# Kernel optimization log

Measured on AMD Instinct MI355X. Metric: run time of the kernel, lower is better.

Reference implementation:

```python
import jax, jax.numpy as jnp
import numpy as np

DIM = 1024
NUM_HEADS = 16
HEAD_DIM = DIM // NUM_HEADS  # 64
LATENT = 128
Q_RANK = 256
B, S = 4, 2048


def setup_inputs() -> dict:
    key = jax.random.key(0)
    ks = jax.random.split(key, 12)
    w = lambda k, shape: jax.random.normal(k, shape, dtype=jnp.float32) * 0.02
    x = jax.random.normal(ks[0], (B, S, DIM), dtype=jnp.float32)
    mask = jnp.tril(jnp.ones((S, S), dtype=jnp.int32))[None, None, :, :]  # causal [1,1,S,S]
    return {
        "x": x,
        "mask": mask,
        "w_kvc": w(ks[1], (DIM, LATENT)),   "b_kvc": jnp.zeros((LATENT,), jnp.float32),
        "w_kvu": w(ks[2], (LATENT, 2 * DIM)), "b_kvu": jnp.zeros((2 * DIM,), jnp.float32),
        "w_qc":  w(ks[3], (DIM, Q_RANK)),   "b_qc": jnp.zeros((Q_RANK,), jnp.float32),
        "w_qu":  w(ks[4], (Q_RANK, DIM)),   "b_qu": jnp.zeros((DIM,), jnp.float32),
        "w_o":   w(ks[5], (DIM, DIM)),      "b_o": jnp.zeros((DIM,), jnp.float32),
    }


def reference(x, mask, w_kvc, b_kvc, w_kvu, b_kvu, w_qc, b_qc, w_qu, b_qu, w_o, b_o):
    b, s, _ = x.shape
    # low-rank KV path
    kv_latent = x @ w_kvc + b_kvc                      # [B,S,latent]
    kv_up = kv_latent @ w_kvu + b_kvu                  # [B,S,2*dim]
    K, V = jnp.split(kv_up, 2, axis=-1)                # each [B,S,dim]
    # low-rank Q path
    Q = (x @ w_qc + b_qc) @ w_qu + b_qu                # [B,S,dim]

    def split_heads(t):  # [B,S,dim] -> [B,H,S,hd]
        return t.reshape(b, s, NUM_HEADS, HEAD_DIM).transpose(0, 2, 1, 3)

    Qh, Kh, Vh = split_heads(Q), split_heads(K), split_heads(V)
    scores = jnp.einsum("bhsd,bhtd->bhst", Qh, Kh) / np.sqrt(HEAD_DIM).astype(np.float32)
    scores = jnp.where(mask == 0, jnp.float32(-1e9), scores)
    attn = jax.nn.softmax(scores, axis=-1)
    ctx = jnp.einsum("bhst,bhtd->bhsd", attn, Vh)      # [B,H,S,hd]
    ctx = ctx.transpose(0, 2, 1, 3).reshape(b, s, DIM)
    return ctx @ w_o + b_o
```

## Files before the change

kernel.cpp:

```cpp
#include <hip/hip_runtime.h>

typedef __attribute__((ext_vector_type(8))) short short8;
typedef __attribute__((ext_vector_type(4))) float f32x4;

#define DIM 1024
#define NH 16
#define HD 64
#define LAT 128
#define QR 256
#define NCAT (LAT + QR)
#define BB 4
#define SS 2048
#define BS (BB * SS)

#define SCALE_LOG2E 0.18033688011112042f

__device__ __forceinline__ unsigned short f2b(float f) {
  unsigned int u = __builtin_bit_cast(unsigned int, f);
  u += 0x7FFFu + ((u >> 16) & 1u);
  return (unsigned short)(u >> 16);
}
__device__ __forceinline__ float b2f(unsigned short h) {
  unsigned int u = ((unsigned int)h) << 16;
  return __builtin_bit_cast(float, u);
}
__device__ __forceinline__ unsigned int pack_bf16_pair(float f0, float f1) {
  unsigned int u0 = __builtin_bit_cast(unsigned int, f0) + 0x8000u;
  unsigned int u1 = __builtin_bit_cast(unsigned int, f1) + 0x8000u;
  return __builtin_amdgcn_perm(u1, u0, 0x07060302u);
}
__device__ __forceinline__ void gll16(const unsigned short* g, unsigned short* l) {
  __builtin_amdgcn_global_load_lds(
      (const __attribute__((address_space(1))) unsigned int*)g,
      (__attribute__((address_space(3))) unsigned int*)l, 16, 0, 0);
}

__global__ __launch_bounds__(256) void cvt_x(const float* __restrict__ in,
                                             unsigned short* __restrict__ out, int n4) {
  int i = blockIdx.x * 256 + threadIdx.x;
  if (i >= n4) return;
  f32x4 v = ((const f32x4*)in)[i];
  ushort4 o;
  o.x = f2b(v[0]); o.y = f2b(v[1]); o.z = f2b(v[2]); o.w = f2b(v[3]);
  ((ushort4*)out)[i] = o;
}

__global__ __launch_bounds__(256) void prep_weights(
    const float* __restrict__ w_kvc, const float* __restrict__ w_qc,
    const float* __restrict__ w_kvu, const float* __restrict__ w_qu,
    const float* __restrict__ w_o, const float* __restrict__ b_kvc,
    const float* __restrict__ b_qc, unsigned short* __restrict__ wcatT,
    unsigned short* __restrict__ wkvuT, unsigned short* __restrict__ wquT,
    unsigned short* __restrict__ woT, float* __restrict__ bias_cat) {
  __shared__ unsigned short T[64 * 72];
  const int id = blockIdx.x;
  const int tid = threadIdx.x;
  if (id >= 480) {
    if (tid < LAT) bias_cat[tid] = b_kvc[tid];
    else bias_cat[tid] = b_qc[tid - LAT];
    if (tid < 128) bias_cat[tid + 256] = b_qc[tid + 128];
    return;
  }
  const float* in; unsigned short* out; int K, N, tile;
  if (id < 32)       { in = w_kvc; out = wcatT;                       K = DIM; N = LAT;     tile = id; }
  else if (id < 96)  { in = w_qc;  out = wcatT + (size_t)LAT * DIM;   K = DIM; N = QR;      tile = id - 32; }
  else if (id < 160) { in = w_kvu; out = wkvuT;                       K = LAT; N = 2 * DIM; tile = id - 96; }
  else if (id < 224) { in = w_qu;  out = wquT;                        K = QR;  N = DIM;     tile = id - 160; }
  else               { in = w_o;   out = woT;                         K = DIM; N = DIM;     tile = id - 224; }
  const int ktiles = K >> 6;
  const int k0 = (tile % ktiles) * 64, n0 = (tile / ktiles) * 64;
  {
    const int r = tid >> 2, cq = (tid & 3) * 16;
#pragma unroll
    for (int j = 0; j < 4; ++j) {
      f32x4 v = *(const f32x4*)(in + (size_t)(k0 + r) * N + n0 + cq + j * 4);
      ushort4 o;
      o.x = f2b(v[0]); o.y = f2b(v[1]); o.z = f2b(v[2]); o.w = f2b(v[3]);
      *(ushort4*)(T + r * 72 + cq + j * 4) = o;
    }
  }
  __syncthreads();
#pragma unroll
  for (int s = 0; s < 2; ++s) {
    int idx = tid + s * 256;
    int nr = idx >> 3, kg = (idx & 7) * 8;
    short8 o;
#pragma unroll
    for (int i = 0; i < 8; i++) o[i] = T[(kg + i) * 72 + nr];
    *(short8*)(out + (size_t)(n0 + nr) * K + k0 + kg) = o;
  }
}

__global__ __launch_bounds__(256) void transpose_v(const unsigned short* __restrict__ KVb,
                                                   unsigned short* __restrict__ VTb) {
  __shared__ unsigned short T[64 * 72];
  const int tid = threadIdx.x;
  const int st = blockIdx.x, dt = blockIdx.y, b = blockIdx.z;
  const int s0 = st * 64, d0 = dt * 64;
#pragma unroll
  for (int t = 0; t < 2; ++t) {
    int idx = tid + t * 256;
    int r = idx >> 3, c = idx & 7;
    short8 v = *(const short8*)(KVb + (size_t)(b * SS + s0 + r) * (2 * DIM) + DIM + d0 + c * 8);
    *(short8*)(T + r * 72 + c * 8) = v;
  }
  __syncthreads();
#pragma unroll
  for (int t = 0; t < 2; ++t) {
    int idx = tid + t * 256;
    int dr = idx >> 3, cg = idx & 7;
    short8 o;
#pragma unroll
    for (int i = 0; i < 8; i++) o[i] = T[(cg * 8 + i) * 72 + dr];
    *(short8*)(VTb + (size_t)(b * DIM + d0 + dr) * SS + s0 + cg * 8) = o;
  }
}

__global__ __launch_bounds__(256, 4) void gemm_lds(const unsigned short* __restrict__ A,
                                                   const unsigned short* __restrict__ WT,
                                                   const float* __restrict__ bias,
                                                   float* __restrict__ outF,
                                                   unsigned short* __restrict__ outB,
                                                   int N, int K, int lda, int ldout,
                                                   float scale, int nblk) {
  __shared__ unsigned short As[128 * 64];
  __shared__ unsigned short Bs[128 * 64];
  const int tid = threadIdx.x;
  const int wave = tid >> 6, lane = tid & 63;
  const int ln = lane & 15, quad = lane >> 4;
  const int chunk = nblk >> 3;
  const int sw = (blockIdx.x & 7) * chunk + (blockIdx.x >> 3);
  const int nwx = N >> 7;
  const int bx = sw % nwx, by = sw / nwx;
  const int m0 = by * 128, n0 = bx * 128;
  const int wm = (wave >> 1) * 64, wn = (wave & 1) * 64;

  const int srow = wave * 32 + (lane >> 3);
  const int scol = (lane & 7) * 8;
  const unsigned short* Ag = A + (size_t)(m0 + srow) * lda + scol;
  const unsigned short* Bg = WT + (size_t)(n0 + srow) * K + scol;
  unsigned short* Al = As + wave * 32 * 64;
  unsigned short* Bl = Bs + wave * 32 * 64;

  f32x4 acc[4][4];
#pragma unroll
  for (int i = 0; i < 4; i++)
#pragma unroll
    for (int j = 0; j < 4; j++) acc[i][j] = (f32x4){0.f, 0.f, 0.f, 0.f};

  for (int k0 = 0; k0 < K; k0 += 64) {
    __syncthreads();
#pragma unroll
    for (int i = 0; i < 4; i++) {
      gll16(Ag + (size_t)i * 8 * lda + k0, Al + i * 8 * 64);
      gll16(Bg + (size_t)i * 8 * K + k0, Bl + i * 8 * 64);
    }
    __syncthreads();
#pragma unroll
    for (int kc = 0; kc < 2; kc++) {
      short8 af[4], bf[4];
#pragma unroll
      for (int i = 0; i < 4; i++) {
        af[i] = *(const short8*)(As + (wm + i * 16 + ln) * 64 + kc * 32 + quad * 8);
        bf[i] = *(const short8*)(Bs + (wn + i * 16 + ln) * 64 + kc * 32 + quad * 8);
      }
#pragma unroll
      for (int mi = 0; mi < 4; mi++)
#pragma unroll
        for (int ni = 0; ni < 4; ni++)
          acc[mi][ni] =
              __builtin_amdgcn_mfma_f32_16x16x32_bf16(af[mi], bf[ni], acc[mi][ni], 0, 0, 0);
    }
  }

#pragma unroll
  for (int mi = 0; mi < 4; mi++) {
    const int row = m0 + wm + mi * 16 + quad * 4;
#pragma unroll
    for (int ni = 0; ni < 4; ni++) {
      const int col = n0 + wn + ni * 16 + ln;
      const float bv = bias[col];
#pragma unroll
      for (int r = 0; r < 4; r++) {
        float v = (acc[mi][ni][r] + bv) * scale;
        size_t o = (size_t)(row + r) * ldout + col;
        if (outF) outF[o] = v;
        if (outB) outB[o] = f2b(v);
      }
    }
  }
}

__global__ __launch_bounds__(256, 4) void attn_mfma(const unsigned short* __restrict__ Qb,
                                                    const unsigned short* __restrict__ KVb,
                                                    const unsigned short* __restrict__ VTb,
                                                    unsigned short* __restrict__ ctxB) {
  __shared__ unsigned short smem[(64 + 64) * 72 + 4 * 16 * 72];
  unsigned short* Ks = smem;
  unsigned short* Vts = smem + 64 * 72;
  unsigned short* Ps = smem + 128 * 72;
  const int tid = threadIdx.x;
  const int wave = tid >> 6, lane = tid & 63;
  const int ln = lane & 15, quad = lane >> 4;
  const int hw = blockIdx.x;
  const int xcd = hw & 7, slot = hw >> 3;
  const int grp = xcd * 8 + (slot >> 4);
  const int pair = slot & 15;
  const int h = grp & 15, b = grp >> 4;
  const int tA = pair, tB = 31 - pair;
  const int s0A = tA * 64, s0B = tB * 64;
  const int ktmaxB = tB;
  const int qminA = s0A + wave * 16, qmaxA = qminA + 15;
  const int qminB = s0B + wave * 16, qmaxB = qminB + 15;

  short8 qfA[2], qfB[2];
  {
    const unsigned short* qa =
        Qb + (size_t)(b * SS + s0A + wave * 16 + ln) * DIM + h * HD + quad * 8;
    qfA[0] = *(const short8*)qa;
    qfA[1] = *(const short8*)(qa + 32);
    const unsigned short* qb2 =
        Qb + (size_t)(b * SS + s0B + wave * 16 + ln) * DIM + h * HD + quad * 8;
    qfB[0] = *(const short8*)qb2;
    qfB[1] = *(const short8*)(qb2 + 32);
  }

  f32x4 ocA[4], ocB[4];
  float lpA = 0.f, lpB = 0.f;
#pragma unroll
  for (int i = 0; i < 4; i++) {
    ocA[i] = (f32x4){0.f, 0.f, 0.f, 0.f};
    ocB[i] = (f32x4){0.f, 0.f, 0.f, 0.f};
  }

  unsigned short* Pw = Ps + wave * (16 * 72);

  const int srow = tid >> 3, sc8 = (tid & 7) * 8;

  const unsigned short* kptr =
      KVb + (size_t)(b * SS + srow) * (2 * DIM) + h * HD + sc8;
  const unsigned short* vptr = VTb + (size_t)(b * DIM + h * HD + srow) * SS + sc8;
  const size_t kstep = (size_t)64 * 2 * DIM;
  const size_t krow32 = (size_t)32 * 2 * DIM;
  const size_t vrow32 = (size_t)32 * SS;

  short8 kreg0 = *(const short8*)kptr;
  short8 kreg1 = *(const short8*)(kptr + krow32);
  short8 vreg0 = *(const short8*)vptr;
  short8 vreg1 = *(const short8*)(vptr + vrow32);

  for (int kt = 0; kt <= ktmaxB; ++kt) {
    __syncthreads();
    *(short8*)(Ks + srow * 72 + sc8) = kreg0;
    *(short8*)(Ks + (srow + 32) * 72 + sc8) = kreg1;
    *(short8*)(Vts + srow * 72 + sc8) = vreg0;
    *(short8*)(Vts + (srow + 32) * 72 + sc8) = vreg1;
    __syncthreads();
    if (kt < ktmaxB) {
      kptr += kstep; vptr += 64;
      kreg0 = *(const short8*)kptr;
      kreg1 = *(const short8*)(kptr + krow32);
      vreg0 = *(const short8*)vptr;
      vreg1 = *(const short8*)(vptr + vrow32);
    }

    const int k0g = kt * 64;

    auto stream = [&](const short8* qf, f32x4* oc, float& lp, const int qminw,
                      const int qmaxw) {
      if (k0g > qmaxw) return;
      const bool needmask = (k0g + 63 > qminw);

      f32x4 sacc[4];
#pragma unroll
      for (int nt = 0; nt < 4; nt++) sacc[nt] = (f32x4){0.f, 0.f, 0.f, 0.f};
      __builtin_amdgcn_s_setprio(1);
#pragma unroll
      for (int kc = 0; kc < 2; kc++) {
#pragma unroll
        for (int nt = 0; nt < 4; nt++) {
          if (k0g + nt * 16 > qmaxw) continue;
          short8 kfrag = *(const short8*)(Ks + (nt * 16 + ln) * 72 + kc * 32 + quad * 8);
          sacc[nt] =
              __builtin_amdgcn_mfma_f32_16x16x32_bf16(kfrag, qf[kc], sacc[nt], 0, 0, 0);
        }
      }
      __builtin_amdgcn_s_setprio(0);

      const int qg = qminw + ln;
      float lt = 0.f;
      if (!needmask) {
#pragma unroll
        for (int nt = 0; nt < 4; nt++) {
          float p0 = __builtin_exp2f(sacc[nt][0]);
          float p1 = __builtin_exp2f(sacc[nt][1]);
          float p2 = __builtin_exp2f(sacc[nt][2]);
          float p3 = __builtin_exp2f(sacc[nt][3]);
          uint2 pw;
          pw.x = pack_bf16_pair(p0, p1);
          pw.y = pack_bf16_pair(p2, p3);
          *(uint2*)(Pw + ln * 72 + nt * 16 + quad * 4) = pw;
          lt += (p0 + p1) + (p2 + p3);
        }
      } else {
#pragma unroll
        for (int nt = 0; nt < 4; nt++) {
          const int base = k0g + nt * 16 + quad * 4;
          float pe[4];
#pragma unroll
          for (int r = 0; r < 4; r++) {
            float p = __builtin_exp2f(sacc[nt][r]);
            if (base + r > qg) p = 0.f;
            pe[r] = p;
          }
          uint2 pw;
          pw.x = pack_bf16_pair(pe[0], pe[1]);
          pw.y = pack_bf16_pair(pe[2], pe[3]);
          *(uint2*)(Pw + ln * 72 + nt * 16 + quad * 4) = pw;
          lt += (pe[0] + pe[1]) + (pe[2] + pe[3]);
        }
      }
      lp += lt;

      __builtin_amdgcn_s_setprio(1);
#pragma unroll
      for (int kc = 0; kc < 2; kc++) {
        if (k0g + kc * 32 > qmaxw) continue;
        short8 pfrag = *(const short8*)(Pw + ln * 72 + kc * 32 + quad * 8);
#pragma unroll
        for (int dt = 0; dt < 4; dt++) {
          short8 vfrag = *(const short8*)(Vts + (dt * 16 + ln) * 72 + kc * 32 + quad * 8);
          oc[dt] =
              __builtin_amdgcn_mfma_f32_16x16x32_bf16(pfrag, vfrag, oc[dt], 0, 0, 0);
        }
      }
      __builtin_amdgcn_s_setprio(0);
    };

    stream(qfA, ocA, lpA, qminA, qmaxA);
    stream(qfB, ocB, lpB, qminB, qmaxB);
  }

  lpA += __shfl_xor(lpA, 16, 64);
  lpA += __shfl_xor(lpA, 32, 64);
  lpB += __shfl_xor(lpB, 16, 64);
  lpB += __shfl_xor(lpB, 32, 64);
  float liA[4], liB[4];
#pragma unroll
  for (int r = 0; r < 4; r++) {
    liA[r] = 1.f / __shfl(lpA, quad * 4 + r, 64);
    liB[r] = 1.f / __shfl(lpB, quad * 4 + r, 64);
  }

  __syncthreads();
#pragma unroll
  for (int r = 0; r < 4; r++) {
#pragma unroll
    for (int dt = 0; dt < 4; dt++)
      smem[(wave * 16 + quad * 4 + r) * 72 + dt * 16 + ln] = f2b(ocA[dt][r] * liA[r]);
  }
  __syncthreads();
#pragma unroll
  for (int t = 0; t < 2; ++t) {
    int idx = tid + t * 256;
    int row = idx >> 3, c = idx & 7;
    short8 v = *(const short8*)(smem + row * 72 + c * 8);
    *(short8*)(ctxB + (size_t)(b * SS + s0A + row) * DIM + h * HD + c * 8) = v;
  }
  __syncthreads();
#pragma unroll
  for (int r = 0; r < 4; r++) {
#pragma unroll
    for (int dt = 0; dt < 4; dt++)
      smem[(wave * 16 + quad * 4 + r) * 72 + dt * 16 + ln] = f2b(ocB[dt][r] * liB[r]);
  }
  __syncthreads();
#pragma unroll
  for (int t = 0; t < 2; ++t) {
    int idx = tid + t * 256;
    int row = idx >> 3, c = idx & 7;
    short8 v = *(const short8*)(smem + row * 72 + c * 8);
    *(short8*)(ctxB + (size_t)(b * SS + s0B + row) * DIM + h * HD + c * 8) = v;
  }
}

extern "C" void kernel_launch(void* const* d_in, const int* in_sizes, int n_in,
                              void* d_out, int out_size, void* d_ws, size_t ws_size,
                              hipStream_t stream) {
  const float* x     = (const float*)d_in[0];
  const float* w_kvc = (const float*)d_in[2];
  const float* b_kvc = (const float*)d_in[3];
  const float* w_kvu = (const float*)d_in[4];
  const float* b_kvu = (const float*)d_in[5];
  const float* w_qc  = (const float*)d_in[6];
  const float* b_qc  = (const float*)d_in[7];
  const float* w_qu  = (const float*)d_in[8];
  const float* b_qu  = (const float*)d_in[9];
  const float* w_o   = (const float*)d_in[10];
  const float* b_o   = (const float*)d_in[11];
  float* out = (float*)d_out;

  unsigned short* xb     = (unsigned short*)d_ws;
  unsigned short* wcatT  = xb + (size_t)BS * DIM;
  unsigned short* wkvuT  = wcatT + (size_t)NCAT * DIM;
  unsigned short* wquT   = wkvuT + (size_t)LAT * 2 * DIM;
  unsigned short* woT    = wquT + (size_t)QR * DIM;
  unsigned short* kvqlat = woT + (size_t)DIM * DIM;
  unsigned short* kvup   = kvqlat + (size_t)BS * NCAT;
  unsigned short* Qbuf   = kvup + (size_t)BS * 2 * DIM;
  unsigned short* ctx    = Qbuf + (size_t)BS * DIM;
  float* bias_cat        = (float*)(ctx + (size_t)BS * DIM);

  cvt_x<<<(BS * DIM / 4 + 255) / 256, 256, 0, stream>>>(x, xb, BS * DIM / 4);
  prep_weights<<<481, 256, 0, stream>>>(w_kvc, w_qc, w_kvu, w_qu, w_o, b_kvc, b_qc,
                                        wcatT, wkvuT, wquT, woT, bias_cat);

  gemm_lds<<<dim3(BS / 128 * (NCAT / 128)), 256, 0, stream>>>(
      xb, wcatT, bias_cat, nullptr, kvqlat, NCAT, DIM, DIM, NCAT, 1.0f,
      BS / 128 * (NCAT / 128));
  gemm_lds<<<dim3(BS / 128 * (2 * DIM / 128)), 256, 0, stream>>>(
      kvqlat, wkvuT, b_kvu, nullptr, kvup, 2 * DIM, LAT, NCAT, 2 * DIM, 1.0f,
      BS / 128 * (2 * DIM / 128));
  unsigned short* VT = xb;
  transpose_v<<<dim3(SS / 64, DIM / 64, BB), 256, 0, stream>>>(kvup, VT);
  gemm_lds<<<dim3(BS / 128 * (DIM / 128)), 256, 0, stream>>>(
      kvqlat + LAT, wquT, b_qu, nullptr, Qbuf, DIM, QR, NCAT, DIM, SCALE_LOG2E,
      BS / 128 * (DIM / 128));
  attn_mfma<<<dim3(32 * NH * BB / 2), 256, 0, stream>>>(Qbuf, kvup, VT, ctx);
  gemm_lds<<<dim3(BS / 128 * (DIM / 128)), 256, 0, stream>>>(
      ctx, woT, b_o, out, nullptr, DIM, DIM, DIM, DIM, 1.0f,
      BS / 128 * (DIM / 128));
}
```

Baseline: 278.8 us.

## Fuse V transpose into KV-up GEMM epilogue, interleave attention streams, swizzle LDS

The KV up-projection GEMM now writes V already transposed through shared memory in its epilogue, which removes the separate transpose kernel and its extra read and write of V. The attention kernel interleaves the two query tiles so each K and V fragment read from LDS feeds the MFMAs of both tiles. It also replaces padded LDS rows with an XOR-swizzled 64-wide layout to cut memory footprint and bank conflicts. Risks are higher register pressure from holding both score tiles at once, and the V half of the KV buffer is no longer written row-major (only the K half is read afterwards).

```diff
diff --git a/kernel.cpp b/kernel.cpp
--- a/kernel.cpp
+++ b/kernel.cpp
@@ -91,40 +91,17 @@
   }
 }
 
-__global__ __launch_bounds__(256) void transpose_v(const unsigned short* __restrict__ KVb,
-                                                   unsigned short* __restrict__ VTb) {
-  __shared__ unsigned short T[64 * 72];
-  const int tid = threadIdx.x;
-  const int st = blockIdx.x, dt = blockIdx.y, b = blockIdx.z;
-  const int s0 = st * 64, d0 = dt * 64;
-#pragma unroll
-  for (int t = 0; t < 2; ++t) {
-    int idx = tid + t * 256;
-    int r = idx >> 3, c = idx & 7;
-    short8 v = *(const short8*)(KVb + (size_t)(b * SS + s0 + r) * (2 * DIM) + DIM + d0 + c * 8);
-    *(short8*)(T + r * 72 + c * 8) = v;
-  }
-  __syncthreads();
-#pragma unroll
-  for (int t = 0; t < 2; ++t) {
-    int idx = tid + t * 256;
-    int dr = idx >> 3, cg = idx & 7;
-    short8 o;
-#pragma unroll
-    for (int i = 0; i < 8; i++) o[i] = T[(cg * 8 + i) * 72 + dr];
-    *(short8*)(VTb + (size_t)(b * DIM + d0 + dr) * SS + s0 + cg * 8) = o;
-  }
-}
-
 __global__ __launch_bounds__(256, 4) void gemm_lds(const unsigned short* __restrict__ A,
                                                    const unsigned short* __restrict__ WT,
                                                    const float* __restrict__ bias,
                                                    float* __restrict__ outF,
                                                    unsigned short* __restrict__ outB,
+                                                   unsigned short* __restrict__ vtOut,
                                                    int N, int K, int lda, int ldout,
                                                    float scale, int nblk) {
-  __shared__ unsigned short As[128 * 64];
-  __shared__ unsigned short Bs[128 * 64];
+  __shared__ unsigned short gsm[17408];
+  unsigned short* As = gsm;
+  unsigned short* Bs = gsm + 8192;
   const int tid = threadIdx.x;
   const int wave = tid >> 6, lane = tid & 63;
   const int ln = lane & 15, quad = lane >> 4;
@@ -173,6 +150,32 @@
     }
   }
 
+  if (vtOut && n0 >= DIM) {
+    __syncthreads();
+#pragma unroll
+    for (int mi = 0; mi < 4; mi++) {
+      const int s = wm + mi * 16 + quad * 4;
+#pragma unroll
+      for (int ni = 0; ni < 4; ni++) {
+        const int d = wn + ni * 16 + ln;
+        const float bv = bias[n0 + d];
+#pragma unroll
+        for (int r = 0; r < 4; r++)
+          gsm[d * 136 + s + r] = f2b(acc[mi][ni][r] + bv);
+      }
+    }
+    __syncthreads();
+    const int d0 = n0 - DIM, bb = m0 >> 11, s0l = m0 & (SS - 1);
+#pragma unroll
+    for (int t = 0; t < 8; ++t) {
+      int idx = tid + t * 256;
+      int dr = idx >> 4, cs = (idx & 15) * 8;
+      short8 v = *(const short8*)(gsm + dr * 136 + cs);
+      *(short8*)(vtOut + (size_t)(bb * DIM + d0 + dr) * SS + s0l + cs) = v;
+    }
+    return;
+  }
+
 #pragma unroll
   for (int mi = 0; mi < 4; mi++) {
     const int row = m0 + wm + mi * 16 + quad * 4;
@@ -195,10 +198,11 @@
                                                     const unsigned short* __restrict__ KVb,
                                                     const unsigned short* __restrict__ VTb,
                                                     unsigned short* __restrict__ ctxB) {
-  __shared__ unsigned short smem[(64 + 64) * 72 + 4 * 16 * 72];
+  __shared__ unsigned short smem[16384];
   unsigned short* Ks = smem;
-  unsigned short* Vts = smem + 64 * 72;
-  unsigned short* Ps = smem + 128 * 72;
+  unsigned short* Vts = smem + 4096;
+  unsigned short* PsA = smem + 8192;
+  unsigned short* PsB = smem + 12288;
   const int tid = threadIdx.x;
   const int wave = tid >> 6, lane = tid & 63;
   const int ln = lane & 15, quad = lane >> 4;
@@ -233,9 +237,12 @@
     ocB[i] = (f32x4){0.f, 0.f, 0.f, 0.f};
   }
 
-  unsigned short* Pw = Ps + wave * (16 * 72);
+  unsigned short* PwA = PsA + wave * (16 * 64);
+  unsigned short* PwB = PsB + wave * (16 * 64);
+  const int swz = (ln & 7) << 3;
 
   const int srow = tid >> 3, sc8 = (tid & 7) * 8;
+  const int ssc = sc8 ^ ((srow & 7) << 3);
 
   const unsigned short* kptr =
       KVb + (size_t)(b * SS + srow) * (2 * DIM) + h * HD + sc8;
@@ -251,10 +258,10 @@
 
   for (int kt = 0; kt <= ktmaxB; ++kt) {
     __syncthreads();
-    *(short8*)(Ks + srow * 72 + sc8) = kreg0;
-    *(short8*)(Ks + (srow + 32) * 72 + sc8) = kreg1;
-    *(short8*)(Vts + srow * 72 + sc8) = vreg0;
-    *(short8*)(Vts + (srow + 32) * 72 + sc8) = vreg1;
+    *(short8*)(Ks + srow * 64 + ssc) = kreg0;
+    *(short8*)(Ks + (srow + 32) * 64 + ssc) = kreg1;
+    *(short8*)(Vts + srow * 64 + ssc) = vreg0;
+    *(short8*)(Vts + (srow + 32) * 64 + ssc) = vreg1;
     __syncthreads();
     if (kt < ktmaxB) {
       kptr += kstep; vptr += 64;
@@ -265,41 +272,45 @@
     }
 
     const int k0g = kt * 64;
-
-    auto stream = [&](const short8* qf, f32x4* oc, float& lp, const int qminw,
-                      const int qmaxw) {
-      if (k0g > qmaxw) return;
-      const bool needmask = (k0g + 63 > qminw);
-
-      f32x4 sacc[4];
-#pragma unroll
-      for (int nt = 0; nt < 4; nt++) sacc[nt] = (f32x4){0.f, 0.f, 0.f, 0.f};
-      __builtin_amdgcn_s_setprio(1);
-#pragma unroll
-      for (int kc = 0; kc < 2; kc++) {
-#pragma unroll
-        for (int nt = 0; nt < 4; nt++) {
-          if (k0g + nt * 16 > qmaxw) continue;
-          short8 kfrag = *(const short8*)(Ks + (nt * 16 + ln) * 72 + kc * 32 + quad * 8);
-          sacc[nt] =
-              __builtin_amdgcn_mfma_f32_16x16x32_bf16(kfrag, qf[kc], sacc[nt], 0, 0, 0);
-        }
-      }
-      __builtin_amdgcn_s_setprio(0);
-
-      const int qg = qminw + ln;
+    const bool aAct = (k0g <= qmaxA);
+
+    f32x4 sA[4], sB[4];
+#pragma unroll
+    for (int nt = 0; nt < 4; nt++) {
+      sA[nt] = (f32x4){0.f, 0.f, 0.f, 0.f};
+      sB[nt] = (f32x4){0.f, 0.f, 0.f, 0.f};
+    }
+    __builtin_amdgcn_s_setprio(1);
+#pragma unroll
+    for (int kc = 0; kc < 2; kc++) {
+      const int rc = (kc * 32 + quad * 8) ^ swz;
+#pragma unroll
+      for (int nt = 0; nt < 4; nt++) {
+        if (k0g + nt * 16 > qmaxB) continue;
+        short8 kfrag = *(const short8*)(Ks + (nt * 16 + ln) * 64 + rc);
+        sB[nt] = __builtin_amdgcn_mfma_f32_16x16x32_bf16(kfrag, qfB[kc], sB[nt], 0, 0, 0);
+        if (aAct && k0g + nt * 16 <= qmaxA)
+          sA[nt] = __builtin_amdgcn_mfma_f32_16x16x32_bf16(kfrag, qfA[kc], sA[nt], 0, 0, 0);
+      }
+    }
+    __builtin_amdgcn_s_setprio(0);
+
+    const int pcs = (ln & 7) << 3;
+    {
+      const bool needmask = (k0g + 63 > qminB);
+      const int qg = qminB + ln;
       float lt = 0.f;
       if (!needmask) {
 #pragma unroll
         for (int nt = 0; nt < 4; nt++) {
-          float p0 = __builtin_exp2f(sacc[nt][0]);
-          float p1 = __builtin_exp2f(sacc[nt][1]);
-          float p2 = __builtin_exp2f(sacc[nt][2]);
-          float p3 = __builtin_exp2f(sacc[nt][3]);
+          float p0 = __builtin_exp2f(sB[nt][0]);
+          float p1 = __builtin_exp2f(sB[nt][1]);
+          float p2 = __builtin_exp2f(sB[nt][2]);
+          float p3 = __builtin_exp2f(sB[nt][3]);
           uint2 pw;
           pw.x = pack_bf16_pair(p0, p1);
           pw.y = pack_bf16_pair(p2, p3);
-          *(uint2*)(Pw + ln * 72 + nt * 16 + quad * 4) = pw;
+          *(uint2*)(PwB + ln * 64 + ((nt * 16 + quad * 4) ^ pcs)) = pw;
           lt += (p0 + p1) + (p2 + p3);
         }
       } else {
@@ -309,36 +320,76 @@
           float pe[4];
 #pragma unroll
           for (int r = 0; r < 4; r++) {
-            float p = __builtin_exp2f(sacc[nt][r]);
+            float p = __builtin_exp2f(sB[nt][r]);
             if (base + r > qg) p = 0.f;
             pe[r] = p;
           }
           uint2 pw;
           pw.x = pack_bf16_pair(pe[0], pe[1]);
           pw.y = pack_bf16_pair(pe[2], pe[3]);
-          *(uint2*)(Pw + ln * 72 + nt * 16 + quad * 4) = pw;
+          *(uint2*)(PwB + ln * 64 + ((nt * 16 + quad * 4) ^ pcs)) = pw;
           lt += (pe[0] + pe[1]) + (pe[2] + pe[3]);
         }
       }
-      lp += lt;
-
-      __builtin_amdgcn_s_setprio(1);
-#pragma unroll
-      for (int kc = 0; kc < 2; kc++) {
-        if (k0g + kc * 32 > qmaxw) continue;
-        short8 pfrag = *(const short8*)(Pw + ln * 72 + kc * 32 + quad * 8);
-#pragma unroll
-        for (int dt = 0; dt < 4; dt++) {
-          short8 vfrag = *(const short8*)(Vts + (dt * 16 + ln) * 72 + kc * 32 + quad * 8);
-          oc[dt] =
-              __builtin_amdgcn_mfma_f32_16x16x32_bf16(pfrag, vfrag, oc[dt], 0, 0, 0);
+      lpB += lt;
+    }
+    if (aAct) {
+      const bool needmask = (k0g + 63 > qminA);
+      const int qg = qminA + ln;
+      float lt = 0.f;
+      if (!needmask) {
+#pragma unroll
+        for (int nt = 0; nt < 4; nt++) {
+          float p0 = __builtin_exp2f(sA[nt][0]);
+          float p1 = __builtin_exp2f(sA[nt][1]);
+          float p2 = __builtin_exp2f(sA[nt][2]);
+          float p3 = __builtin_exp2f(sA[nt][3]);
+          uint2 pw;
+          pw.x = pack_bf16_pair(p0, p1);
+          pw.y = pack_bf16_pair(p2, p3);
+          *(uint2*)(PwA + ln * 64 + ((nt * 16 + quad * 4) ^ pcs)) = pw;
+          lt += (p0 + p1) + (p2 + p3);
         }
-      }
-      __builtin_amdgcn_s_setprio(0);
-    };
-
-    stream(qfA, ocA, lpA, qminA, qmaxA);
-    stream(qfB, ocB, lpB, qminB, qmaxB);
+      } else {
+#pragma unroll
+        for (int nt = 0; nt < 4; nt++) {
+          const int base = k0g + nt * 16 + quad * 4;
+          float pe[4];
+#pragma unroll
+          for (int r = 0; r < 4; r++) {
+            float p = __builtin_exp2f(sA[nt][r]);
+            if (base + r > qg) p = 0.f;
+            pe[r] = p;
+          }
+          uint2 pw;
+          pw.x = pack_bf16_pair(pe[0], pe[1]);
+          pw.y = pack_bf16_pair(pe[2], pe[3]);
+          *(uint2*)(PwA + ln * 64 + ((nt * 16 + quad * 4) ^ pcs)) = pw;
+          lt += (pe[0] + pe[1]) + (pe[2] + pe[3]);
+        }
+      }
+      lpA += lt;
+    }
+
+    __builtin_amdgcn_s_setprio(1);
+#pragma unroll
+    for (int kc = 0; kc < 2; kc++) {
+      const bool bPV = (k0g + kc * 32 <= qmaxB);
+      const bool aPV = aAct && (k0g + kc * 32 <= qmaxA);
+      if (!bPV) continue;
+      const int rc = (kc * 32 + quad * 8) ^ swz;
+      short8 pB = *(const short8*)(PwB + ln * 64 + rc);
+      short8 pA;
+      if (aPV) pA = *(const short8*)(PwA + ln * 64 + rc);
+#pragma unroll
+      for (int dt = 0; dt < 4; dt++) {
+        short8 vfrag = *(const short8*)(Vts + (dt * 16 + ln) * 64 + rc);
+        ocB[dt] = __builtin_amdgcn_mfma_f32_16x16x32_bf16(pB, vfrag, ocB[dt], 0, 0, 0);
+        if (aPV)
+          ocA[dt] = __builtin_amdgcn_mfma_f32_16x16x32_bf16(pA, vfrag, ocA[dt], 0, 0, 0);
+      }
+    }
+    __builtin_amdgcn_s_setprio(0);
   }
 
   lpA += __shfl_xor(lpA, 16, 64);
@@ -416,18 +467,17 @@
                                         wcatT, wkvuT, wquT, woT, bias_cat);
 
   gemm_lds<<<dim3(BS / 128 * (NCAT / 128)), 256, 0, stream>>>(
-      xb, wcatT, bias_cat, nullptr, kvqlat, NCAT, DIM, DIM, NCAT, 1.0f,
+      xb, wcatT, bias_cat, nullptr, kvqlat, nullptr, NCAT, DIM, DIM, NCAT, 1.0f,
       BS / 128 * (NCAT / 128));
+  unsigned short* VT = xb;
   gemm_lds<<<dim3(BS / 128 * (2 * DIM / 128)), 256, 0, stream>>>(
-      kvqlat, wkvuT, b_kvu, nullptr, kvup, 2 * DIM, LAT, NCAT, 2 * DIM, 1.0f,
+      kvqlat, wkvuT, b_kvu, nullptr, kvup, VT, 2 * DIM, LAT, NCAT, 2 * DIM, 1.0f,
       BS / 128 * (2 * DIM / 128));
-  unsigned short* VT = xb;
-  transpose_v<<<dim3(SS / 64, DIM / 64, BB), 256, 0, stream>>>(kvup, VT);
   gemm_lds<<<dim3(BS / 128 * (DIM / 128)), 256, 0, stream>>>(
-      kvqlat + LAT, wquT, b_qu, nullptr, Qbuf, DIM, QR, NCAT, DIM, SCALE_LOG2E,
+      kvqlat + LAT, wquT, b_qu, nullptr, Qbuf, nullptr, DIM, QR, NCAT, DIM, SCALE_LOG2E,
       BS / 128 * (DIM / 128));
   attn_mfma<<<dim3(32 * NH * BB / 2), 256, 0, stream>>>(Qbuf, kvup, VT, ctx);
   gemm_lds<<<dim3(BS / 128 * (DIM / 128)), 256, 0, stream>>>(
-      ctx, woT, b_o, out, nullptr, DIM, DIM, DIM, DIM, 1.0f,
+      ctx, woT, b_o, out, nullptr, nullptr, DIM, DIM, DIM, DIM, 1.0f,
       BS / 128 * (DIM / 128));
 }
```

Measured after the change: 577.9 us. 2.07x slower.

## Fuse V transpose into KV up-projection epilogue and swizzle attention LDS layout

Applied to the files above, without the earlier changes.

The KV up-projection GEMM now writes V tiles straight out in transposed layout through an LDS staging buffer in its epilogue, so the separate transpose_v kernel and its extra read of V from global memory are gone. V columns are no longer written to kvup, which is safe because attention reads V only from VT. The attention kernel also replaces padded LDS rows (stride 72) with unpadded rows (stride 64) plus an XOR swizzle on K, V and P tiles, shrinking shared memory while trying to avoid bank conflicts. The GEMM's shared-memory footprint grows to fit the transpose staging tile, which may reduce occupancy slightly.

```diff
diff --git a/kernel.cpp b/kernel.cpp
--- a/kernel.cpp
+++ b/kernel.cpp
@@ -91,40 +91,17 @@
   }
 }
 
-__global__ __launch_bounds__(256) void transpose_v(const unsigned short* __restrict__ KVb,
-                                                   unsigned short* __restrict__ VTb) {
-  __shared__ unsigned short T[64 * 72];
-  const int tid = threadIdx.x;
-  const int st = blockIdx.x, dt = blockIdx.y, b = blockIdx.z;
-  const int s0 = st * 64, d0 = dt * 64;
-#pragma unroll
-  for (int t = 0; t < 2; ++t) {
-    int idx = tid + t * 256;
-    int r = idx >> 3, c = idx & 7;
-    short8 v = *(const short8*)(KVb + (size_t)(b * SS + s0 + r) * (2 * DIM) + DIM + d0 + c * 8);
-    *(short8*)(T + r * 72 + c * 8) = v;
-  }
-  __syncthreads();
-#pragma unroll
-  for (int t = 0; t < 2; ++t) {
-    int idx = tid + t * 256;
-    int dr = idx >> 3, cg = idx & 7;
-    short8 o;
-#pragma unroll
-    for (int i = 0; i < 8; i++) o[i] = T[(cg * 8 + i) * 72 + dr];
-    *(short8*)(VTb + (size_t)(b * DIM + d0 + dr) * SS + s0 + cg * 8) = o;
-  }
-}
-
 __global__ __launch_bounds__(256, 4) void gemm_lds(const unsigned short* __restrict__ A,
                                                    const unsigned short* __restrict__ WT,
                                                    const float* __restrict__ bias,
                                                    float* __restrict__ outF,
                                                    unsigned short* __restrict__ outB,
+                                                   unsigned short* __restrict__ vtOut,
                                                    int N, int K, int lda, int ldout,
                                                    float scale, int nblk) {
-  __shared__ unsigned short As[128 * 64];
-  __shared__ unsigned short Bs[128 * 64];
+  __shared__ unsigned short gsm[17408];
+  unsigned short* As = gsm;
+  unsigned short* Bs = gsm + 8192;
   const int tid = threadIdx.x;
   const int wave = tid >> 6, lane = tid & 63;
   const int ln = lane & 15, quad = lane >> 4;
@@ -173,6 +150,32 @@
     }
   }
 
+  if (vtOut && n0 >= DIM) {
+    __syncthreads();
+#pragma unroll
+    for (int mi = 0; mi < 4; mi++) {
+      const int s = wm + mi * 16 + quad * 4;
+#pragma unroll
+      for (int ni = 0; ni < 4; ni++) {
+        const int d = wn + ni * 16 + ln;
+        const float bv = bias[n0 + d];
+#pragma unroll
+        for (int r = 0; r < 4; r++)
+          gsm[d * 136 + s + r] = f2b(acc[mi][ni][r] + bv);
+      }
+    }
+    __syncthreads();
+    const int d0 = n0 - DIM, bb = m0 >> 11, s0l = m0 & (SS - 1);
+#pragma unroll
+    for (int t = 0; t < 8; ++t) {
+      int idx = tid + t * 256;
+      int dr = idx >> 4, cs = (idx & 15) * 8;
+      short8 v = *(const short8*)(gsm + dr * 136 + cs);
+      *(short8*)(vtOut + (size_t)(bb * DIM + d0 + dr) * SS + s0l + cs) = v;
+    }
+    return;
+  }
+
 #pragma unroll
   for (int mi = 0; mi < 4; mi++) {
     const int row = m0 + wm + mi * 16 + quad * 4;
@@ -195,10 +198,10 @@
                                                     const unsigned short* __restrict__ KVb,
                                                     const unsigned short* __restrict__ VTb,
                                                     unsigned short* __restrict__ ctxB) {
-  __shared__ unsigned short smem[(64 + 64) * 72 + 4 * 16 * 72];
+  __shared__ unsigned short smem[12288];
   unsigned short* Ks = smem;
-  unsigned short* Vts = smem + 64 * 72;
-  unsigned short* Ps = smem + 128 * 72;
+  unsigned short* Vts = smem + 4096;
+  unsigned short* Ps = smem + 8192;
   const int tid = threadIdx.x;
   const int wave = tid >> 6, lane = tid & 63;
   const int ln = lane & 15, quad = lane >> 4;
@@ -233,9 +236,11 @@
     ocB[i] = (f32x4){0.f, 0.f, 0.f, 0.f};
   }
 
-  unsigned short* Pw = Ps + wave * (16 * 72);
+  unsigned short* Pw = Ps + wave * (16 * 64);
+  const int swz = (ln & 7) << 3;
 
   const int srow = tid >> 3, sc8 = (tid & 7) * 8;
+  const int ssc = sc8 ^ ((srow & 7) << 3);
 
   const unsigned short* kptr =
       KVb + (size_t)(b * SS + srow) * (2 * DIM) + h * HD + sc8;
@@ -251,10 +256,10 @@
 
   for (int kt = 0; kt <= ktmaxB; ++kt) {
     __syncthreads();
-    *(short8*)(Ks + srow * 72 + sc8) = kreg0;
-    *(short8*)(Ks + (srow + 32) * 72 + sc8) = kreg1;
-    *(short8*)(Vts + srow * 72 + sc8) = vreg0;
-    *(short8*)(Vts + (srow + 32) * 72 + sc8) = vreg1;
+    *(short8*)(Ks + srow * 64 + ssc) = kreg0;
+    *(short8*)(Ks + (srow + 32) * 64 + ssc) = kreg1;
+    *(short8*)(Vts + srow * 64 + ssc) = vreg0;
+    *(short8*)(Vts + (srow + 32) * 64 + ssc) = vreg1;
     __syncthreads();
     if (kt < ktmaxB) {
       kptr += kstep; vptr += 64;
@@ -277,10 +282,11 @@
       __builtin_amdgcn_s_setprio(1);
 #pragma unroll
       for (int kc = 0; kc < 2; kc++) {
+        const int rc = (kc * 32 + quad * 8) ^ swz;
 #pragma unroll
         for (int nt = 0; nt < 4; nt++) {
           if (k0g + nt * 16 > qmaxw) continue;
-          short8 kfrag = *(const short8*)(Ks + (nt * 16 + ln) * 72 + kc * 32 + quad * 8);
+          short8 kfrag = *(const short8*)(Ks + (nt * 16 + ln) * 64 + rc);
           sacc[nt] =
               __builtin_amdgcn_mfma_f32_16x16x32_bf16(kfrag, qf[kc], sacc[nt], 0, 0, 0);
         }
@@ -299,7 +305,7 @@
           uint2 pw;
           pw.x = pack_bf16_pair(p0, p1);
           pw.y = pack_bf16_pair(p2, p3);
-          *(uint2*)(Pw + ln * 72 + nt * 16 + quad * 4) = pw;
+          *(uint2*)(Pw + ln * 64 + ((nt * 16 + quad * 4) ^ swz)) = pw;
           lt += (p0 + p1) + (p2 + p3);
         }
       } else {
@@ -316,7 +322,7 @@
           uint2 pw;
           pw.x = pack_bf16_pair(pe[0], pe[1]);
           pw.y = pack_bf16_pair(pe[2], pe[3]);
-          *(uint2*)(Pw + ln * 72 + nt * 16 + quad * 4) = pw;
+          *(uint2*)(Pw + ln * 64 + ((nt * 16 + quad * 4) ^ swz)) = pw;
           lt += (pe[0] + pe[1]) + (pe[2] + pe[3]);
         }
       }
@@ -326,10 +332,11 @@
 #pragma unroll
       for (int kc = 0; kc < 2; kc++) {
         if (k0g + kc * 32 > qmaxw) continue;
-        short8 pfrag = *(const short8*)(Pw + ln * 72 + kc * 32 + quad * 8);
+        const int rc = (kc * 32 + quad * 8) ^ swz;
+        short8 pfrag = *(const short8*)(Pw + ln * 64 + rc);
 #pragma unroll
         for (int dt = 0; dt < 4; dt++) {
-          short8 vfrag = *(const short8*)(Vts + (dt * 16 + ln) * 72 + kc * 32 + quad * 8);
+          short8 vfrag = *(const short8*)(Vts + (dt * 16 + ln) * 64 + rc);
           oc[dt] =
               __builtin_amdgcn_mfma_f32_16x16x32_bf16(pfrag, vfrag, oc[dt], 0, 0, 0);
         }
@@ -416,18 +423,17 @@
                                         wcatT, wkvuT, wquT, woT, bias_cat);
 
   gemm_lds<<<dim3(BS / 128 * (NCAT / 128)), 256, 0, stream>>>(
-      xb, wcatT, bias_cat, nullptr, kvqlat, NCAT, DIM, DIM, NCAT, 1.0f,
+      xb, wcatT, bias_cat, nullptr, kvqlat, nullptr, NCAT, DIM, DIM, NCAT, 1.0f,
       BS / 128 * (NCAT / 128));
+  unsigned short* VT = xb;
   gemm_lds<<<dim3(BS / 128 * (2 * DIM / 128)), 256, 0, stream>>>(
-      kvqlat, wkvuT, b_kvu, nullptr, kvup, 2 * DIM, LAT, NCAT, 2 * DIM, 1.0f,
+      kvqlat, wkvuT, b_kvu, nullptr, kvup, VT, 2 * DIM, LAT, NCAT, 2 * DIM, 1.0f,
       BS / 128 * (2 * DIM / 128));
-  unsigned short* VT = xb;
-  transpose_v<<<dim3(SS / 64, DIM / 64, BB), 256, 0, stream>>>(kvup, VT);
   gemm_lds<<<dim3(BS / 128 * (DIM / 128)), 256, 0, stream>>>(
-      kvqlat + LAT, wquT, b_qu, nullptr, Qbuf, DIM, QR, NCAT, DIM, SCALE_LOG2E,
+      kvqlat + LAT, wquT, b_qu, nullptr, Qbuf, nullptr, DIM, QR, NCAT, DIM, SCALE_LOG2E,
       BS / 128 * (DIM / 128));
   attn_mfma<<<dim3(32 * NH * BB / 2), 256, 0, stream>>>(Qbuf, kvup, VT, ctx);
   gemm_lds<<<dim3(BS / 128 * (DIM / 128)), 256, 0, stream>>>(
-      ctx, woT, b_o, out, nullptr, DIM, DIM, DIM, DIM, 1.0f,
+      ctx, woT, b_o, out, nullptr, nullptr, DIM, DIM, DIM, DIM, 1.0f,
       BS / 128 * (DIM / 128));
 }
```

Result: faster. 267.0 us (-4.2%).
